# Kernel optimization log

Measured on AMD Instinct MI355X. Metric: run time of the kernel, lower is better.

## Reference

```python
import jax, jax.numpy as jnp
import numpy as np

# Model dims (see init_kwargs / shape_source)
B = 2048      # batch
CIN = 256     # tabular input features (c_in)
NH = 512      # TabularEncoder hidden width
NENC_HID = 4  # nlayers=6 -> input layer + 4 hidden + output layer
NF = 112      # n_features = num_concepts (conv=False path)
K = 112       # num_concepts
NL = 50       # num_latent_concepts
MC = 100      # num_monte_carlo
NOUT = 200    # num_output


def setup_inputs() -> dict:
    key = jax.random.key(0)
    ks = jax.random.split(key, 8)
    x = jax.random.normal(ks[0], (B, CIN), dtype=jnp.float32)
    enc_Win = jax.random.normal(ks[1], (CIN, NH), dtype=jnp.float32) * (1.0 / np.sqrt(CIN))
    enc_bin = jnp.zeros((NH,), jnp.float32)
    enc_Wh = jax.random.normal(ks[2], (NENC_HID, NH, NH), dtype=jnp.float32) * (1.0 / np.sqrt(NH))
    enc_bh = jnp.zeros((NENC_HID, NH), jnp.float32)
    enc_Wout = jax.random.normal(ks[3], (NH, NF), dtype=jnp.float32) * (1.0 / np.sqrt(NH))
    enc_bout = jnp.zeros((NF,), jnp.float32)
    # Per-concept predictor i has first Linear of shape [NF+i, NL]; pad all to [NF+K, NL]
    # and statically slice rows [:NF+i] in the loop (unused padded rows never touched).
    pred_W1 = jax.random.normal(ks[4], (K, NF + K, NL), dtype=jnp.float32) * (1.0 / np.sqrt(NF))
    pred_b1 = jnp.zeros((K, NL), jnp.float32)
    pred_W2 = jax.random.normal(ks[5], (K, NL), dtype=jnp.float32) * (1.0 / np.sqrt(NL))
    pred_b2 = jnp.zeros((K,), jnp.float32)
    head_W = jax.random.normal(ks[6], (K, NOUT), dtype=jnp.float32) * (1.0 / np.sqrt(K))
    head_b = jnp.zeros((NOUT,), jnp.float32)
    return {
        "x": x,
        "enc_Win": enc_Win, "enc_bin": enc_bin,
        "enc_Wh": enc_Wh, "enc_bh": enc_bh,
        "enc_Wout": enc_Wout, "enc_bout": enc_bout,
        "pred_W1": pred_W1, "pred_b1": pred_b1,
        "pred_W2": pred_W2, "pred_b2": pred_b2,
        "head_W": head_W, "head_b": head_b,
        "epoch": 0,
    }


def reference(x, enc_Win, enc_bin, enc_Wh, enc_bh, enc_Wout, enc_bout,
              pred_W1, pred_b1, pred_W2, pred_b2, head_W, head_b, epoch):
    lrelu = jax.nn.leaky_relu  # negative_slope=0.01, matches nn.LeakyReLU default

    # ---- TabularEncoder (ni=CIN, nhidden=NH, nlayers=6, no=NF) ----
    h = lrelu(x @ enc_Win + enc_bin)
    for i in range(enc_Wh.shape[0]):
        h = lrelu(h @ enc_Wh[i] + enc_bh[i])
    inter = h @ enc_Wout + enc_bout                      # [B, NF]
    Bn = inter.shape[0]

    key = jax.random.key(42)
    c_hard = jnp.zeros((Bn, K, MC), inter.dtype)
    c_probs = []
    for i in range(K):
        W1 = pred_W1[i, :NF + i]                          # [NF+i, NL]
        base = inter @ W1[:NF] + pred_b1[i]               # [B, NL], shared across MC
        if i == 0:
            p1 = jax.nn.sigmoid(lrelu(base) @ pred_W2[i] + pred_b2[i])   # [B]
            p = jnp.broadcast_to(p1[:, None], (Bn, MC))   # expand(-1,-1,MC)
        else:
            # add contribution of the i previously sampled hard concepts, per MC sample
            hpre = base[:, None, :] + jnp.einsum('bim,ih->bmh', c_hard[:, :i], W1[NF:])  # [B,MC,NL]
            p = jax.nn.sigmoid(jnp.einsum('bmh,h->bm', lrelu(hpre), pred_W2[i]) + pred_b2[i])  # [B,MC]
        key, sk = jax.random.split(key)
        samp = jax.random.bernoulli(sk, p).astype(p.dtype)  # torch.bernoulli(concept)
        c_hard = c_hard.at[:, i, :].set(samp)
        c_probs.append(p)

    c_prob = jnp.stack(c_probs, axis=1)                   # [B, K, MC]

    # ---- Head: MC average of softmax probabilities (pred_dim > 1 branch) ----
    logits = jnp.einsum('bkm,ko->bmo', c_hard, head_W) + head_b   # [B, MC, NOUT]
    probs = jax.nn.softmax(logits, axis=-1).mean(axis=1)          # [B, NOUT]
    y_pred_logits = jnp.log(probs + 1e-6)
    return (c_prob, y_pred_logits, c_hard)
```

## Files before the change

### kernel.cpp

```cpp
#include <hip/hip_runtime.h>

typedef unsigned int u32;
typedef unsigned short u16;
typedef unsigned long long u64;

#define YOFF  22937600ull
#define CHOFF 23347200ull

#define OFF_HA    0ull
#define OFF_HB    4194304ull
#define OFF_INTER 8388608ull

__host__ __device__ inline u32 rotl32_(u32 x, int r) { return (x << r) | (x >> (32 - r)); }
__host__ __device__ inline void tf2x32(u32 k0, u32 k1, u32 c0, u32 c1, u32& o0, u32& o1) {
  u32 ks0 = k0, ks1 = k1, ks2 = k0 ^ k1 ^ 0x1BD11BDAu;
  u32 x0 = c0 + ks0, x1 = c1 + ks1;
  const int RA[4] = {13, 15, 26, 6}, RB[4] = {17, 29, 16, 24};
  for (int i = 0; i < 5; ++i) {
    const int* R = (i & 1) ? RB : RA;
    for (int j = 0; j < 4; ++j) { x0 += x1; x1 = rotl32_(x1, R[j]); x1 ^= x0; }
    switch (i) {
      case 0: x0 += ks1; x1 += ks2 + 1u; break;
      case 1: x0 += ks2; x1 += ks0 + 2u; break;
      case 2: x0 += ks0; x1 += ks1 + 3u; break;
      case 3: x0 += ks1; x1 += ks2 + 4u; break;
      case 4: x0 += ks2; x1 += ks0 + 5u; break;
    }
  }
  o0 = x0; o1 = x1;
}

struct SKeys { u32 v[224]; };

template <bool DO_LRELU>
__global__ __launch_bounds__(256) void gemm_bias(const float* __restrict__ A,
                                                 const float* __restrict__ Bm,
                                                 const float* __restrict__ bias,
                                                 float* __restrict__ C,
                                                 int M, int N, int K) {
  __shared__ float As[32][33];
  __shared__ float Bs[32][65];
  const int bm = blockIdx.y * 32, bn = blockIdx.x * 64;
  const int t = threadIdx.x;
  const int ty = t >> 4, tx = t & 15;
  float acc[2][4] = {};
  for (int k0 = 0; k0 < K; k0 += 32) {
    {
      int e = t;
      int m = e >> 3, k4 = e & 7;
      float4 v = *(const float4*)(A + (size_t)(bm + m) * K + (k0 + k4 * 4));
      As[k4 * 4 + 0][m] = v.x; As[k4 * 4 + 1][m] = v.y;
      As[k4 * 4 + 2][m] = v.z; As[k4 * 4 + 3][m] = v.w;
    }
#pragma unroll
    for (int l = 0; l < 2; ++l) {
      int e = l * 256 + t;
      int k = e >> 4, n4 = e & 15;
      int gn = bn + n4 * 4;
      if (gn < N) {
        float4 v = *(const float4*)(Bm + (size_t)(k0 + k) * N + gn);
        Bs[k][n4 * 4 + 0] = v.x; Bs[k][n4 * 4 + 1] = v.y;
        Bs[k][n4 * 4 + 2] = v.z; Bs[k][n4 * 4 + 3] = v.w;
      } else {
        Bs[k][n4 * 4 + 0] = 0.f; Bs[k][n4 * 4 + 1] = 0.f;
        Bs[k][n4 * 4 + 2] = 0.f; Bs[k][n4 * 4 + 3] = 0.f;
      }
    }
    __syncthreads();
#pragma unroll
    for (int kk = 0; kk < 32; ++kk) {
      float a[2], b[4];
#pragma unroll
      for (int j = 0; j < 2; ++j) a[j] = As[kk][ty * 2 + j];
#pragma unroll
      for (int j = 0; j < 4; ++j) b[j] = Bs[kk][tx * 4 + j];
#pragma unroll
      for (int i = 0; i < 2; ++i)
#pragma unroll
        for (int j = 0; j < 4; ++j) acc[i][j] = fmaf(a[i], b[j], acc[i][j]);
    }
    __syncthreads();
  }
#pragma unroll
  for (int i = 0; i < 2; ++i) {
#pragma unroll
    for (int j = 0; j < 4; ++j) {
      int m = bm + ty * 2 + i, n = bn + tx * 4 + j;
      if (n < N) {
        float s = acc[i][j] + bias[n];
        if (DO_LRELU) { if (s < 0.f) s = 0.01f * s; }
        C[(size_t)m * N + n] = s;
      }
    }
  }
}

__global__ __launch_bounds__(256) void base_kernel(const float* __restrict__ inter,
                                                   const float* __restrict__ W1,
                                                   const float* __restrict__ pb1,
                                                   float* __restrict__ out) {
  __shared__ float As[112][65];
  __shared__ float Ws[112][64];
  const int i = blockIdx.y;
  const int b0 = blockIdx.x * 64;
  const int t = threadIdx.x;
  const int ty = t >> 4, tx = t & 15;
#pragma unroll
  for (int l = 0; l < 7; ++l) {
    int e4 = l * 256 + t;
    int k4 = e4 % 28, bs = e4 / 28;
    float4 v = *(const float4*)(inter + (size_t)(b0 + bs) * 112 + k4 * 4);
    As[k4 * 4 + 0][bs] = v.x; As[k4 * 4 + 1][bs] = v.y;
    As[k4 * 4 + 2][bs] = v.z; As[k4 * 4 + 3][bs] = v.w;
  }
#pragma unroll
  for (int l = 0; l < 28; ++l) {
    int e = l * 256 + t;
    int r = e >> 6, c = e & 63;
    Ws[r][c] = (c < 50) ? W1[(size_t)i * 11200 + r * 50 + c] : 0.f;
  }
  __syncthreads();
  float acc[4][4] = {};
  for (int kk = 0; kk < 112; ++kk) {
    float a[4], b[4];
#pragma unroll
    for (int j = 0; j < 4; ++j) { a[j] = As[kk][ty * 4 + j]; b[j] = Ws[kk][tx * 4 + j]; }
#pragma unroll
    for (int ii = 0; ii < 4; ++ii)
#pragma unroll
      for (int j = 0; j < 4; ++j) acc[ii][j] = fmaf(a[ii], b[j], acc[ii][j]);
  }
#pragma unroll
  for (int ii = 0; ii < 4; ++ii) {
#pragma unroll
    for (int j = 0; j < 4; ++j) {
      int b = b0 + ty * 4 + ii, h = tx * 4 + j;
      if (h < 50) {
        out[CHOFF + (size_t)b * 11200 + (size_t)i * 100 + h] = acc[ii][j] + pb1[i * 50 + h];
      }
    }
  }
}

__global__ __launch_bounds__(128, 4) void sample_team(const float* __restrict__ W1,
                                                      const float* __restrict__ W2,
                                                      const float* __restrict__ b2v,
                                                      float* __restrict__ out,
                                                      u32* __restrict__ masks, SKeys sks) {
  __shared__ float vbuf[2][64][28];
  const int t = threadIdx.x;
  const int lane = t & 63;
  const int subu = __builtin_amdgcn_readfirstlane(t >> 6);
  const int p = blockIdx.x * 64 + lane;
  const int b = p / 100;
  const int m = p - b * 100;
  const float* __restrict__ baserow = out + CHOFF + (size_t)b * 11200 + subu * 25;
  u64 lo = 0, hi = 0;
  float acc[25], pv[25];

  for (int i = 0; i < 112; ++i) {
#pragma unroll
    for (int h = 0; h < 25; ++h) acc[h] = 0.f;
    {
      const float* __restrict__ Wi = W1 + (size_t)i * 11200 + 5600 + subu * 25;
      int r = 0;
      for (; r + 1 < i; r += 2) {
        float cA = (((r < 64) ? (lo >> r) : (hi >> (r - 64))) & 1ull) ? 1.f : 0.f;
        int r2 = r + 1;
        float cB = (((r2 < 64) ? (lo >> r2) : (hi >> (r2 - 64))) & 1ull) ? 1.f : 0.f;
        const float* __restrict__ wA = Wi + (size_t)r * 50;
#pragma unroll
        for (int h = 0; h < 25; ++h)
          acc[h] = fmaf(cB, wA[50 + h], fmaf(cA, wA[h], acc[h]));
      }
      if (r < i) {
        float cA = (((r < 64) ? (lo >> r) : (hi >> (r - 64))) & 1ull) ? 1.f : 0.f;
        const float* __restrict__ wA = Wi + (size_t)r * 50;
#pragma unroll
        for (int h = 0; h < 25; ++h) acc[h] = fmaf(cA, wA[h], acc[h]);
      }
    }
    {
      const float* bs = baserow + (size_t)i * 100;
#pragma unroll
      for (int h = 0; h < 25; ++h) {
        float x = acc[h] + bs[h];
        acc[h] = (x < 0.f) ? 0.01f * x : x;
      }
    }
#pragma unroll
    for (int h = 0; h < 25; ++h) vbuf[subu][lane][h] = acc[h];
    __syncthreads();
#pragma unroll
    for (int h = 0; h < 25; ++h) pv[h] = vbuf[1 - subu][lane][h];
    __syncthreads();
    const float* __restrict__ w2 = W2 + i * 50;
    float s = 0.f;
    if (subu == 0) {
#pragma unroll
      for (int h = 0; h < 25; ++h) s = fmaf(acc[h], w2[h], s);
#pragma unroll
      for (int h = 0; h < 25; ++h) s = fmaf(pv[h], w2[25 + h], s);
    } else {
#pragma unroll
      for (int h = 0; h < 25; ++h) s = fmaf(pv[h], w2[h], s);
#pragma unroll
      for (int h = 0; h < 25; ++h) s = fmaf(acc[h], w2[25 + h], s);
    }
    float l = s + b2v[i];
    float pr = 1.f / (1.f + expf(-l));
    u32 a0, a1;
    tf2x32(sks.v[2 * i], sks.v[2 * i + 1], 0u, (u32)p, a0, a1);
    u32 fb = ((a0 ^ a1) >> 9) | 0x3F800000u;
    float uu; __builtin_memcpy(&uu, &fb, 4); uu -= 1.f;
    u64 sbit = (uu < pr) ? 1ull : 0ull;
    if (subu == 0) out[(size_t)b * 11200 + (size_t)i * 100 + m] = pr;
    if (i < 64) lo |= sbit << i; else hi |= sbit << (i - 64);
  }
  if (subu == 0) {
    u32* mp = masks + (size_t)p * 4;
    mp[0] = (u32)lo; mp[1] = (u32)(lo >> 32);
    mp[2] = (u32)hi; mp[3] = (u32)(hi >> 32);
  }
}

__global__ __launch_bounds__(256) void expand_kernel(const u32* __restrict__ masks,
                                                     float* __restrict__ out) {
  __shared__ u32 mW[100][4];
  const int b = blockIdx.x;
  const int t = threadIdx.x;
  if (t < 100) {
    const u32* mp = masks + ((size_t)b * 100 + t) * 4;
    mW[t][0] = mp[0]; mW[t][1] = mp[1]; mW[t][2] = mp[2]; mW[t][3] = mp[3];
  }
  __syncthreads();
  for (int e = t; e < 11200; e += 256) {
    int i = e / 100, m = e - i * 100;
    u32 word = mW[m][i >> 5];
    out[CHOFF + (size_t)b * 11200 + e] = (float)((word >> (i & 31)) & 1u);
  }
}

__global__ __launch_bounds__(256) void head_kernel(const float* __restrict__ HW,
                                                   const float* __restrict__ hb,
                                                   float* __restrict__ out) {
  __shared__ unsigned char cS[100][116];
  __shared__ float lgS[50][201];
  const int b = blockIdx.x;
  const int t = threadIdx.x;
  for (int e = t; e < 11200; e += 256) {
    int k = e / 100, m = e - k * 100;
    cS[m][k] = (out[CHOFF + (size_t)b * 11200 + (size_t)k * 100 + m] != 0.f) ? 1 : 0;
  }
  __syncthreads();
  float pacc = 0.f;
  for (int mh = 0; mh < 2; ++mh) {
    for (int l = 0; l < 3; ++l) {
      int tile = l * 256 + t;
      if (tile < 625) {
        int o0 = (tile % 25) * 8;
        int m0 = (tile / 25) * 2;
        float acc[2][8] = {};
        for (int k = 0; k < 112; ++k) {
          float4 wa = *(const float4*)(HW + (size_t)k * 200 + o0);
          float4 wb = *(const float4*)(HW + (size_t)k * 200 + o0 + 4);
          float w[8] = {wa.x, wa.y, wa.z, wa.w, wb.x, wb.y, wb.z, wb.w};
          float c0 = (float)cS[mh * 50 + m0][k];
          float c1 = (float)cS[mh * 50 + m0 + 1][k];
#pragma unroll
          for (int jo = 0; jo < 8; ++jo) {
            acc[0][jo] = fmaf(c0, w[jo], acc[0][jo]);
            acc[1][jo] = fmaf(c1, w[jo], acc[1][jo]);
          }
        }
#pragma unroll
        for (int im = 0; im < 2; ++im)
#pragma unroll
          for (int jo = 0; jo < 8; ++jo) {
            int o = o0 + jo;
            lgS[m0 + im][o] = acc[im][jo] + hb[o];
          }
      }
    }
    __syncthreads();
    if (t < 50) {
      int m = t;
      float mx = -3.0e38f;
      for (int o = 0; o < 200; ++o) mx = fmaxf(mx, lgS[m][o]);
      float s = 0.f;
      for (int o = 0; o < 200; ++o) {
        float e = expf(lgS[m][o] - mx);
        lgS[m][o] = e; s += e;
      }
      float inv = 1.f / s;
      for (int o = 0; o < 200; ++o) lgS[m][o] = lgS[m][o] * inv;
    }
    __syncthreads();
    if (t < 200) { for (int m = 0; m < 50; ++m) pacc += lgS[m][t]; }
    __syncthreads();
  }
  if (t < 200) {
    out[YOFF + (size_t)b * 200 + t] = logf(pacc / 100.f + 1e-6f);
  }
}

extern "C" void kernel_launch(void* const* d_in, const int* in_sizes, int n_in,
                              void* d_out, int out_size, void* d_ws, size_t ws_size,
                              hipStream_t stream) {
  const float* x    = (const float*)d_in[0];
  const float* Win  = (const float*)d_in[1];
  const float* bin  = (const float*)d_in[2];
  const float* Wh   = (const float*)d_in[3];
  const float* bh   = (const float*)d_in[4];
  const float* Wout = (const float*)d_in[5];
  const float* bout = (const float*)d_in[6];
  const float* pW1  = (const float*)d_in[7];
  const float* pb1  = (const float*)d_in[8];
  const float* pW2  = (const float*)d_in[9];
  const float* pb2  = (const float*)d_in[10];
  const float* hW   = (const float*)d_in[11];
  const float* hb   = (const float*)d_in[12];
  float* out = (float*)d_out;
  char* ws = (char*)d_ws;

  float* hA     = (float*)(ws + OFF_HA);
  float* hB     = (float*)(ws + OFF_HB);
  float* interB = (float*)(ws + OFF_INTER);
  u32*   masks  = (u32*)(ws + OFF_HB);

  gemm_bias<true ><<<dim3(8, 64), 256, 0, stream>>>(x,  Win,             bin,          hA,     2048, 512, 256);
  gemm_bias<true ><<<dim3(8, 64), 256, 0, stream>>>(hA, Wh + 0 * 262144, bh + 0 * 512, hB,     2048, 512, 512);
  gemm_bias<true ><<<dim3(8, 64), 256, 0, stream>>>(hB, Wh + 1 * 262144, bh + 1 * 512, hA,     2048, 512, 512);
  gemm_bias<true ><<<dim3(8, 64), 256, 0, stream>>>(hA, Wh + 2 * 262144, bh + 2 * 512, hB,     2048, 512, 512);
  gemm_bias<true ><<<dim3(8, 64), 256, 0, stream>>>(hB, Wh + 3 * 262144, bh + 3 * 512, hA,     2048, 512, 512);
  gemm_bias<false><<<dim3(2, 64), 256, 0, stream>>>(hA, Wout,            bout,         interB, 2048, 112, 512);

  base_kernel<<<dim3(32, 112), 256, 0, stream>>>(interB, pW1, pb1, out);

  SKeys sks;
  {
    u32 k0 = 0u, k1 = 42u;
    for (int i = 0; i < 112; ++i) {
      u32 nk0, nk1, s0, s1;
      tf2x32(k0, k1, 0u, 0u, nk0, nk1);
      tf2x32(k0, k1, 0u, 1u, s0, s1);
      sks.v[2 * i] = s0; sks.v[2 * i + 1] = s1;
      k0 = nk0; k1 = nk1;
    }
  }
  sample_team<<<3200, 128, 0, stream>>>(pW1, pW2, pb2, out, masks, sks);
  expand_kernel<<<2048, 256, 0, stream>>>(masks, out);

  head_kernel<<<2048, 256, 0, stream>>>(hW, hb, out);
}
```

Baseline: 3.822 ms.

## Stage predictor W1 rows in double-buffered LDS, one thread per sample

Replaces the two-wave split sampler, which exchanged partial hidden vectors through shared memory and read W1 from global memory, with a kernel where each thread owns all 50 hidden units of one (batch, MC) sample. The W1 rows needed for concept i are loaded through registers into a double-buffered LDS tile and padded to 52 floats so they can be read as float4, and the next concept's rows are prefetched while the current one is computed. This removes the per-step cross-wave exchange and the repeated global weight reads. In exchange each thread holds 50 accumulators plus 22 staging registers, which raises register pressure and lowers occupancy, and a block-wide barrier is still needed every step.

```diff
diff --git a/kernel.cpp b/kernel.cpp
--- a/kernel.cpp
+++ b/kernel.cpp
@@ -142,86 +142,110 @@
   }
 }
 
-__global__ __launch_bounds__(128, 4) void sample_team(const float* __restrict__ W1,
-                                                      const float* __restrict__ W2,
-                                                      const float* __restrict__ b2v,
-                                                      float* __restrict__ out,
-                                                      u32* __restrict__ masks, SKeys sks) {
-  __shared__ float vbuf[2][64][28];
-  const int t = threadIdx.x;
-  const int lane = t & 63;
-  const int subu = __builtin_amdgcn_readfirstlane(t >> 6);
-  const int p = blockIdx.x * 64 + lane;
+#define SROW 52
+#define SBUF (112 * SROW)
+__global__ __launch_bounds__(256, 3) void sample_lds(const float* __restrict__ W1,
+                                                     const float* __restrict__ W2,
+                                                     const float* __restrict__ b2v,
+                                                     float* __restrict__ out,
+                                                     u32* __restrict__ masks, SKeys sks) {
+  __shared__ float wlds[2 * SBUF];
+  const int t = threadIdx.x;
+  const int p = blockIdx.x * 256 + t;
   const int b = p / 100;
   const int m = p - b * 100;
-  const float* __restrict__ baserow = out + CHOFF + (size_t)b * 11200 + subu * 25;
+  const float* __restrict__ baserow = out + CHOFF + (size_t)b * 11200;
   u64 lo = 0, hi = 0;
-  float acc[25], pv[25];
+  float acc[50];
+  float stg[22];
 
   for (int i = 0; i < 112; ++i) {
-#pragma unroll
-    for (int h = 0; h < 25; ++h) acc[h] = 0.f;
+    const int D = (i + 1) * 50;
+    if (i < 111) {
+      const float* __restrict__ Wn = W1 + (size_t)(i + 1) * 11200 + 5600;
+#pragma unroll
+      for (int l = 0; l < 22; ++l) {
+        int e = t + l * 256;
+        if (e < D) stg[l] = Wn[e];
+      }
+    }
+#pragma unroll
+    for (int h = 0; h < 50; ++h) acc[h] = 0.f;
     {
-      const float* __restrict__ Wi = W1 + (size_t)i * 11200 + 5600 + subu * 25;
+      const float* __restrict__ Lb = wlds + (i & 1) * SBUF;
       int r = 0;
-      for (; r + 1 < i; r += 2) {
-        float cA = (((r < 64) ? (lo >> r) : (hi >> (r - 64))) & 1ull) ? 1.f : 0.f;
-        int r2 = r + 1;
-        float cB = (((r2 < 64) ? (lo >> r2) : (hi >> (r2 - 64))) & 1ull) ? 1.f : 0.f;
-        const float* __restrict__ wA = Wi + (size_t)r * 50;
-#pragma unroll
-        for (int h = 0; h < 25; ++h)
-          acc[h] = fmaf(cB, wA[50 + h], fmaf(cA, wA[h], acc[h]));
-      }
-      if (r < i) {
-        float cA = (((r < 64) ? (lo >> r) : (hi >> (r - 64))) & 1ull) ? 1.f : 0.f;
-        const float* __restrict__ wA = Wi + (size_t)r * 50;
-#pragma unroll
-        for (int h = 0; h < 25; ++h) acc[h] = fmaf(cA, wA[h], acc[h]);
+      int r1 = (i < 64) ? i : 64;
+      u64 cm = lo;
+      for (; r < r1; ++r) {
+        float c = (cm & 1ull) ? 1.f : 0.f;
+        cm >>= 1;
+        const float4* __restrict__ w4 = (const float4*)(Lb + r * SROW);
+#pragma unroll
+        for (int j = 0; j < 12; ++j) {
+          float4 q = w4[j];
+          acc[4 * j + 0] = fmaf(c, q.x, acc[4 * j + 0]);
+          acc[4 * j + 1] = fmaf(c, q.y, acc[4 * j + 1]);
+          acc[4 * j + 2] = fmaf(c, q.z, acc[4 * j + 2]);
+          acc[4 * j + 3] = fmaf(c, q.w, acc[4 * j + 3]);
+        }
+        float2 e2 = *(const float2*)(Lb + r * SROW + 48);
+        acc[48] = fmaf(c, e2.x, acc[48]);
+        acc[49] = fmaf(c, e2.y, acc[49]);
+      }
+      cm = hi;
+      for (; r < i; ++r) {
+        float c = (cm & 1ull) ? 1.f : 0.f;
+        cm >>= 1;
+        const float4* __restrict__ w4 = (const float4*)(Lb + r * SROW);
+#pragma unroll
+        for (int j = 0; j < 12; ++j) {
+          float4 q = w4[j];
+          acc[4 * j + 0] = fmaf(c, q.x, acc[4 * j + 0]);
+          acc[4 * j + 1] = fmaf(c, q.y, acc[4 * j + 1]);
+          acc[4 * j + 2] = fmaf(c, q.z, acc[4 * j + 2]);
+          acc[4 * j + 3] = fmaf(c, q.w, acc[4 * j + 3]);
+        }
+        float2 e2 = *(const float2*)(Lb + r * SROW + 48);
+        acc[48] = fmaf(c, e2.x, acc[48]);
+        acc[49] = fmaf(c, e2.y, acc[49]);
       }
     }
     {
+      const float* __restrict__ w2 = W2 + i * 50;
       const float* bs = baserow + (size_t)i * 100;
-#pragma unroll
-      for (int h = 0; h < 25; ++h) {
-        float x = acc[h] + bs[h];
-        acc[h] = (x < 0.f) ? 0.01f * x : x;
-      }
-    }
-#pragma unroll
-    for (int h = 0; h < 25; ++h) vbuf[subu][lane][h] = acc[h];
-    __syncthreads();
-#pragma unroll
-    for (int h = 0; h < 25; ++h) pv[h] = vbuf[1 - subu][lane][h];
-    __syncthreads();
-    const float* __restrict__ w2 = W2 + i * 50;
-    float s = 0.f;
-    if (subu == 0) {
-#pragma unroll
-      for (int h = 0; h < 25; ++h) s = fmaf(acc[h], w2[h], s);
-#pragma unroll
-      for (int h = 0; h < 25; ++h) s = fmaf(pv[h], w2[25 + h], s);
-    } else {
-#pragma unroll
-      for (int h = 0; h < 25; ++h) s = fmaf(pv[h], w2[h], s);
-#pragma unroll
-      for (int h = 0; h < 25; ++h) s = fmaf(acc[h], w2[25 + h], s);
-    }
-    float l = s + b2v[i];
-    float pr = 1.f / (1.f + expf(-l));
-    u32 a0, a1;
-    tf2x32(sks.v[2 * i], sks.v[2 * i + 1], 0u, (u32)p, a0, a1);
-    u32 fb = ((a0 ^ a1) >> 9) | 0x3F800000u;
-    float uu; __builtin_memcpy(&uu, &fb, 4); uu -= 1.f;
-    u64 sbit = (uu < pr) ? 1ull : 0ull;
-    if (subu == 0) out[(size_t)b * 11200 + (size_t)i * 100 + m] = pr;
-    if (i < 64) lo |= sbit << i; else hi |= sbit << (i - 64);
-  }
-  if (subu == 0) {
-    u32* mp = masks + (size_t)p * 4;
-    mp[0] = (u32)lo; mp[1] = (u32)(lo >> 32);
-    mp[2] = (u32)hi; mp[3] = (u32)(hi >> 32);
-  }
+      float s = 0.f;
+#pragma unroll
+      for (int h = 0; h < 50; ++h) {
+        float v = acc[h] + bs[h];
+        if (v < 0.f) v = 0.01f * v;
+        s = fmaf(v, w2[h], s);
+      }
+      float l = s + b2v[i];
+      float pr = 1.f / (1.f + expf(-l));
+      u32 a0, a1;
+      tf2x32(sks.v[2 * i], sks.v[2 * i + 1], 0u, (u32)p, a0, a1);
+      u32 fb = ((a0 ^ a1) >> 9) | 0x3F800000u;
+      float uu; __builtin_memcpy(&uu, &fb, 4); uu -= 1.f;
+      u64 sbit = (uu < pr) ? 1ull : 0ull;
+      out[(size_t)b * 11200 + (size_t)i * 100 + m] = pr;
+      if (i < 64) lo |= sbit << i; else hi |= sbit << (i - 64);
+    }
+    if (i < 111) {
+      float* __restrict__ Ln = wlds + ((i + 1) & 1) * SBUF;
+#pragma unroll
+      for (int l = 0; l < 22; ++l) {
+        int e = t + l * 256;
+        if (e < D) {
+          int r = e / 50, c = e - r * 50;
+          Ln[r * SROW + c] = stg[l];
+        }
+      }
+    }
+    __syncthreads();
+  }
+  u32* mp = masks + (size_t)p * 4;
+  mp[0] = (u32)lo; mp[1] = (u32)(lo >> 32);
+  mp[2] = (u32)hi; mp[3] = (u32)(hi >> 32);
 }
 
 __global__ __launch_bounds__(256) void expand_kernel(const u32* __restrict__ masks,
@@ -348,7 +372,7 @@
       k0 = nk0; k1 = nk1;
     }
   }
-  sample_team<<<3200, 128, 0, stream>>>(pW1, pW2, pb2, out, masks, sks);
+  sample_lds<<<800, 256, 0, stream>>>(pW1, pW2, pb2, out, masks, sks);
   expand_kernel<<<2048, 256, 0, stream>>>(masks, out);
 
   head_kernel<<<2048, 256, 0, stream>>>(hW, hb, out);
```

Measured after the change: 5.995 ms. 56.9% more time.
